# Kernel tuning notes

Measured on AMD Instinct MI355X. Metric: run time of the kernel, lower is better.

## Reference

```python
import jax, jax.numpy as jnp
import numpy as np

EMB_DIM = 128
HEAD_SIZE = 16  # embDim // numHea = 128 // 8


def setup_inputs() -> dict:
    key = jax.random.key(0)
    k1, k2, k3, k4 = jax.random.split(key, 4)
    B, T = 8, 2048
    inpEmb = jax.random.normal(k1, (B, T, EMB_DIM), dtype=jnp.float32)
    # nn.Linear(embDim, heaSiz, bias=False) weights, stored transposed so y = x @ W
    Wq = jax.random.normal(k2, (EMB_DIM, HEAD_SIZE), dtype=jnp.float32) / np.sqrt(EMB_DIM)
    Wk = jax.random.normal(k3, (EMB_DIM, HEAD_SIZE), dtype=jnp.float32) / np.sqrt(EMB_DIM)
    Wv = jax.random.normal(k4, (EMB_DIM, HEAD_SIZE), dtype=jnp.float32) / np.sqrt(EMB_DIM)
    return {"inpEmb": inpEmb, "Wq": Wq, "Wk": Wk, "Wv": Wv}


def reference(inpEmb, Wq, Wk, Wv):
    # q,k,v: [B, T, H]
    q = inpEmb @ Wq
    k = inpEmb @ Wk
    v = inpEmb @ Wv
    scale = HEAD_SIZE ** -0.5
    # scores: [B, T, T]
    scores = jnp.einsum('bqh,bkh->bqk', q, k) * scale
    T = inpEmb.shape[1]
    causal = jnp.tril(jnp.ones((T, T), dtype=bool))
    scores = jnp.where(causal, scores, -jnp.inf)
    weights = jax.nn.softmax(scores, axis=-1)
    # dropout treated as identity (eval mode) for deterministic reference
    return jnp.einsum('bqk,bkh->bqh', weights, v)
```

## Files before the change

kernel.cpp:

```cpp
#include <hip/hip_runtime.h>
#include <hip/hip_bf16.h>

#define T_SEQ 2048
#define EMB   128
#define H     16
#define BATCH 8
#define MAXP  16
#define VSTR  2064
#define SLOT  10
#define QSCALE 0.360673760222241f

#define EXP2F(x) __builtin_amdgcn_exp2f(x)

typedef short short8_t __attribute__((ext_vector_type(8)));
typedef float f32x4    __attribute__((ext_vector_type(4)));

__device__ __forceinline__ unsigned short f2bf(float f) {
    __hip_bfloat16 h = __float2bfloat16(f);
    return *reinterpret_cast<unsigned short*>(&h);
}

__global__ __launch_bounds__(256) void qkv_kernel(
    const float* __restrict__ x,
    const float* __restrict__ Wq,
    const float* __restrict__ Wk,
    const float* __restrict__ Wv,
    unsigned short* __restrict__ Qbf,
    unsigned short* __restrict__ Kbf,
    unsigned short* __restrict__ Vt)
{
    __shared__ unsigned short Wt[3][16][136];

    const int tid = threadIdx.x;
#pragma unroll
    for (int p = 0; p < 6; ++p) {
        const int idx4 = tid + p * 256;
        const int flat = idx4 * 4;
        const int mm   = flat >> 11;
        const int rem  = flat & 2047;
        const int d    = rem >> 4;
        const int c0   = rem & 15;
        const float* Wm = (mm == 0) ? Wq : (mm == 1) ? Wk : Wv;
        float4 w = *reinterpret_cast<const float4*>(Wm + rem);
        Wt[mm][c0    ][d] = f2bf(w.x);
        Wt[mm][c0 + 1][d] = f2bf(w.y);
        Wt[mm][c0 + 2][d] = f2bf(w.z);
        Wt[mm][c0 + 3][d] = f2bf(w.w);
    }
    __syncthreads();

    const int wv   = tid >> 6;
    const int lane = tid & 63;
    const int q    = lane >> 4;
    const int n    = lane & 15;
    const int row0 = blockIdx.x * 64 + wv * 16;
    const float* xr = x + (size_t)(row0 + n) * EMB;

    f32x4 aq = {0,0,0,0}, ak = {0,0,0,0}, av = {0,0,0,0};
#pragma unroll
    for (int t = 0; t < 4; ++t) {
        const int k0 = t * 32 + q * 8;
        float4 xa = *reinterpret_cast<const float4*>(xr + k0);
        float4 xb = *reinterpret_cast<const float4*>(xr + k0 + 4);
        union { unsigned short s[8]; short8_t v; } xf;
        xf.s[0]=f2bf(xa.x); xf.s[1]=f2bf(xa.y); xf.s[2]=f2bf(xa.z); xf.s[3]=f2bf(xa.w);
        xf.s[4]=f2bf(xb.x); xf.s[5]=f2bf(xb.y); xf.s[6]=f2bf(xb.z); xf.s[7]=f2bf(xb.w);
        short8_t wqf = *reinterpret_cast<const short8_t*>(&Wt[0][n][k0]);
        short8_t wkf = *reinterpret_cast<const short8_t*>(&Wt[1][n][k0]);
        short8_t wvf = *reinterpret_cast<const short8_t*>(&Wt[2][n][k0]);
        aq = __builtin_amdgcn_mfma_f32_16x16x32_bf16(xf.v, wqf, aq, 0, 0, 0);
        ak = __builtin_amdgcn_mfma_f32_16x16x32_bf16(xf.v, wkf, ak, 0, 0, 0);
        av = __builtin_amdgcn_mfma_f32_16x16x32_bf16(xf.v, wvf, av, 0, 0, 0);
    }

    const int grow = row0 + q * 4;
    const int b    = grow >> 11;
    const int ib0  = grow & 2047;
#pragma unroll
    for (int r = 0; r < 4; ++r) {
        Qbf[(size_t)(grow + r) * H + n] = f2bf(aq[r] * QSCALE);
        Kbf[(size_t)(grow + r) * H + n] = f2bf(ak[r]);
    }
    union { unsigned short s[4]; unsigned long long u; } vp;
    vp.s[0]=f2bf(av[0]); vp.s[1]=f2bf(av[1]); vp.s[2]=f2bf(av[2]); vp.s[3]=f2bf(av[3]);
    *reinterpret_cast<unsigned long long*>(
        Vt + ((size_t)b * H + n) * VSTR + ib0) = vp.u;
}

__global__ __launch_bounds__(256) void attn_phase1(
    const unsigned short* __restrict__ Qbf,
    const unsigned short* __restrict__ Kbf,
    const unsigned short* __restrict__ Vt,
    unsigned int* __restrict__ P2)
{
    __shared__ unsigned int Pbuf[4][16][68];

    int r = blockIdx.x;
    int qt = 0;
    while (r >= (qt >> 1) + 1) { r -= (qt >> 1) + 1; ++qt; }
    const int cch  = r;
    const int b    = blockIdx.y;
    const int i0   = qt << 6;
    const int j0   = cch << 7;

    const int tid  = threadIdx.x;
    const int wv   = tid >> 6;
    const int lane = tid & 63;
    const int q    = lane >> 4;
    const int n    = lane & 15;
    const int wrow0 = i0 + wv * 16;
    const int irow  = wrow0 + n;

    const unsigned short* Qp = Qbf + (size_t)b * T_SEQ * H;
    const unsigned short* Kp = Kbf + (size_t)b * T_SEQ * H;
    const unsigned short* vrow = Vt + (size_t)b * H * VSTR + (size_t)n * VSTR;

    short8_t qf = {0,0,0,0,0,0,0,0};
    if (q < 2)
        qf = *reinterpret_cast<const short8_t*>(Qp + (size_t)irow * H + q * 8);

    f32x4 S[8];
#pragma unroll
    for (int s = 0; s < 8; ++s) {
        short8_t kf = {0,0,0,0,0,0,0,0};
        if (q < 2)
            kf = *reinterpret_cast<const short8_t*>(
                    Kp + (size_t)(j0 + s * 16 + n) * H + q * 8);
        f32x4 z = {0.f, 0.f, 0.f, 0.f};
        S[s] = __builtin_amdgcn_mfma_f32_16x16x32_bf16(kf, qf, z, 0, 0, 0);
    }
    short8_t vf[4];
#pragma unroll
    for (int h = 0; h < 4; ++h)
        vf[h] = *reinterpret_cast<const short8_t*>(vrow + j0 + h * 32 + q * 8);

    float tm = -1e30f;
    if (j0 + 127 > wrow0) {
#pragma unroll
        for (int s = 0; s < 8; ++s) {
            const int kb = j0 + s * 16 + q * 4;
#pragma unroll
            for (int rr = 0; rr < 4; ++rr) {
                float v = (kb + rr <= irow) ? S[s][rr] : -1e30f;
                S[s][rr] = v;
                tm = fmaxf(tm, v);
            }
        }
    } else {
#pragma unroll
        for (int s = 0; s < 8; ++s)
            tm = fmaxf(tm, fmaxf(fmaxf(S[s][0], S[s][1]),
                                 fmaxf(S[s][2], S[s][3])));
    }
    tm = fmaxf(tm, __shfl_xor(tm, 16));
    tm = fmaxf(tm, __shfl_xor(tm, 32));
    const float m = tm;

    float l = 0.f;
#pragma unroll
    for (int s = 0; s < 8; ++s) {
        float e0 = EXP2F(S[s][0] - m);
        float e1 = EXP2F(S[s][1] - m);
        float e2 = EXP2F(S[s][2] - m);
        float e3 = EXP2F(S[s][3] - m);
        l += (e0 + e1) + (e2 + e3);
        unsigned int b0 = __builtin_bit_cast(unsigned int, e0);
        unsigned int b1 = __builtin_bit_cast(unsigned int, e1);
        unsigned int b2 = __builtin_bit_cast(unsigned int, e2);
        unsigned int b3 = __builtin_bit_cast(unsigned int, e3);
        unsigned long long pw =
            (unsigned long long)((b1 & 0xffff0000u) | (b0 >> 16)) |
            ((unsigned long long)((b3 & 0xffff0000u) | (b2 >> 16)) << 32);
        *reinterpret_cast<unsigned long long*>(&Pbuf[wv][n][8 * s + 2 * q]) = pw;
    }

    f32x4 acc = {0.f, 0.f, 0.f, 0.f};
#pragma unroll
    for (int h = 0; h < 4; ++h) {
        uint4 p4 = *reinterpret_cast<const uint4*>(&Pbuf[wv][n][16 * h + 4 * q]);
        union { uint4 u; short8_t v; } pu; pu.u = p4;
        acc = __builtin_amdgcn_mfma_f32_16x16x32_bf16(vf[h], pu.v, acc, 0, 0, 0);
    }

    l += __shfl_xor(l, 16);
    l += __shfl_xor(l, 32);

    unsigned int* pp = P2 + ((size_t)(b * T_SEQ + irow) * MAXP + cch) * SLOT;
    const unsigned int pa =
        (unsigned int)f2bf(acc[0]) | ((unsigned int)f2bf(acc[1]) << 16);
    const unsigned int pb =
        (unsigned int)f2bf(acc[2]) | ((unsigned int)f2bf(acc[3]) << 16);
    unsigned long long aw = (unsigned long long)pa |
                            ((unsigned long long)pb << 32);
    *reinterpret_cast<unsigned long long*>(pp + 2 * q) = aw;
    if (q == 0) {
        unsigned long long mlw =
            (unsigned long long)__builtin_bit_cast(unsigned int, m) |
            ((unsigned long long)__builtin_bit_cast(unsigned int, l) << 32);
        *reinterpret_cast<unsigned long long*>(pp + 8) = mlw;
    }
}

__global__ __launch_bounds__(256) void attn_phase2(
    const unsigned int* __restrict__ P2, float* __restrict__ out)
{
    const int gid = blockIdx.x * 256 + threadIdx.x;
    const int row = gid >> 4;
    const int d   = gid & 15;
    const int ib  = row & (T_SEQ - 1);
    const int nc  = (ib >> 7) + 1;
    const unsigned int* base = P2 + (size_t)row * (MAXP * SLOT);
    const int dpair = d >> 1;
    const int dhi   = (d & 1) << 4;

    float mv[MAXP];
#pragma unroll
    for (int p = 0; p < MAXP; ++p) {
        const float raw = __builtin_bit_cast(float, base[p * SLOT + 8]);
        mv[p] = (p < nc) ? raw : -1e30f;
    }
    float M = -1e30f;
#pragma unroll
    for (int p = 0; p < MAXP; ++p) M = fmaxf(M, mv[p]);

    float L = 0.f, o = 0.f;
#pragma unroll
    for (int p = 0; p < MAXP; ++p) {
        const float wgt = EXP2F(mv[p] - M);
        const float lv  = __builtin_bit_cast(float, base[p * SLOT + 9]);
        const unsigned int pr = base[p * SLOT + dpair];
        const float av = __builtin_bit_cast(float, ((pr >> dhi) & 0xffffu) << 16);
        L += wgt * lv;
        o += wgt * av;
    }
    out[gid] = o / L;
}

extern "C" void kernel_launch(void* const* d_in, const int* in_sizes, int n_in,
                              void* d_out, int out_size, void* d_ws, size_t ws_size,
                              hipStream_t stream)
{
    const float* x  = (const float*)d_in[0];
    const float* Wq = (const float*)d_in[1];
    const float* Wk = (const float*)d_in[2];
    const float* Wv = (const float*)d_in[3];
    float* out = (float*)d_out;

    const size_t NE = (size_t)BATCH * T_SEQ * H;
    unsigned short* Qbf = (unsigned short*)d_ws;
    unsigned short* Kbf = Qbf + NE;
    unsigned short* Vt  = Kbf + NE;
    unsigned int* P2 = (unsigned int*)(Vt + (size_t)BATCH * H * VSTR);

    qkv_kernel<<<BATCH * T_SEQ / 64, 256, 0, stream>>>(
        x, Wq, Wk, Wv, Qbf, Kbf, Vt);
    attn_phase1<<<dim3(272, BATCH), 256, 0, stream>>>(Qbf, Kbf, Vt, P2);
    attn_phase2<<<(int)(NE / 256), 256, 0, stream>>>(P2, out);
}
```

Baseline: 84.24 us.

## Fuse split-K attention phases into single online-softmax kernel

Replaces the two-kernel attention (per-chunk partials written to workspace, then a merge kernel) with one kernel per 64-row query tile that loops over key chunks using online softmax rescaling. This removes the partial-result workspace traffic and one kernel launch. In exchange the grid shrinks to 256 blocks with causal load imbalance, so later tiles serially process up to 16 chunks, which reduces parallelism.

```diff
diff --git a/kernel.cpp b/kernel.cpp
--- a/kernel.cpp
+++ b/kernel.cpp
@@ -5,9 +5,7 @@
 #define EMB   128
 #define H     16
 #define BATCH 8
-#define MAXP  16
 #define VSTR  2064
-#define SLOT  10
 #define QSCALE 0.360673760222241f
 
 #define EXP2F(x) __builtin_amdgcn_exp2f(x)
@@ -87,21 +85,18 @@
         Vt + ((size_t)b * H + n) * VSTR + ib0) = vp.u;
 }
 
-__global__ __launch_bounds__(256) void attn_phase1(
+__global__ __launch_bounds__(256) void attn_fused(
     const unsigned short* __restrict__ Qbf,
     const unsigned short* __restrict__ Kbf,
     const unsigned short* __restrict__ Vt,
-    unsigned int* __restrict__ P2)
+    float* __restrict__ out)
 {
     __shared__ unsigned int Pbuf[4][16][68];
 
-    int r = blockIdx.x;
-    int qt = 0;
-    while (r >= (qt >> 1) + 1) { r -= (qt >> 1) + 1; ++qt; }
-    const int cch  = r;
-    const int b    = blockIdx.y;
-    const int i0   = qt << 6;
-    const int j0   = cch << 7;
+    const int qt = blockIdx.x;
+    const int b  = blockIdx.y;
+    const int i0 = qt << 6;
+    const int nc = (qt >> 1) + 1;
 
     const int tid  = threadIdx.x;
     const int wv   = tid >> 6;
@@ -119,121 +114,92 @@
     if (q < 2)
         qf = *reinterpret_cast<const short8_t*>(Qp + (size_t)irow * H + q * 8);
 
-    f32x4 S[8];
-#pragma unroll
-    for (int s = 0; s < 8; ++s) {
-        short8_t kf = {0,0,0,0,0,0,0,0};
-        if (q < 2)
-            kf = *reinterpret_cast<const short8_t*>(
-                    Kp + (size_t)(j0 + s * 16 + n) * H + q * 8);
-        f32x4 z = {0.f, 0.f, 0.f, 0.f};
-        S[s] = __builtin_amdgcn_mfma_f32_16x16x32_bf16(kf, qf, z, 0, 0, 0);
-    }
-    short8_t vf[4];
-#pragma unroll
-    for (int h = 0; h < 4; ++h)
-        vf[h] = *reinterpret_cast<const short8_t*>(vrow + j0 + h * 32 + q * 8);
-
-    float tm = -1e30f;
-    if (j0 + 127 > wrow0) {
+    f32x4 acc = {0.f, 0.f, 0.f, 0.f};
+    float m = -1e30f;
+    float l = 0.f;
+
+    for (int c = 0; c < nc; ++c) {
+        const int j0 = c << 7;
+
+        f32x4 S[8];
 #pragma unroll
         for (int s = 0; s < 8; ++s) {
-            const int kb = j0 + s * 16 + q * 4;
-#pragma unroll
-            for (int rr = 0; rr < 4; ++rr) {
-                float v = (kb + rr <= irow) ? S[s][rr] : -1e30f;
-                S[s][rr] = v;
-                tm = fmaxf(tm, v);
+            short8_t kf = {0,0,0,0,0,0,0,0};
+            if (q < 2)
+                kf = *reinterpret_cast<const short8_t*>(
+                        Kp + (size_t)(j0 + s * 16 + n) * H + q * 8);
+            f32x4 z = {0.f, 0.f, 0.f, 0.f};
+            S[s] = __builtin_amdgcn_mfma_f32_16x16x32_bf16(kf, qf, z, 0, 0, 0);
+        }
+        short8_t vf[4];
+#pragma unroll
+        for (int h = 0; h < 4; ++h)
+            vf[h] = *reinterpret_cast<const short8_t*>(vrow + j0 + h * 32 + q * 8);
+
+        float tm = -1e30f;
+        if (j0 + 127 > wrow0) {
+#pragma unroll
+            for (int s = 0; s < 8; ++s) {
+                const int kb = j0 + s * 16 + q * 4;
+#pragma unroll
+                for (int rr = 0; rr < 4; ++rr) {
+                    float v = (kb + rr <= irow) ? S[s][rr] : -1e30f;
+                    S[s][rr] = v;
+                    tm = fmaxf(tm, v);
+                }
             }
-        }
-    } else {
-#pragma unroll
-        for (int s = 0; s < 8; ++s)
-            tm = fmaxf(tm, fmaxf(fmaxf(S[s][0], S[s][1]),
-                                 fmaxf(S[s][2], S[s][3])));
-    }
-    tm = fmaxf(tm, __shfl_xor(tm, 16));
-    tm = fmaxf(tm, __shfl_xor(tm, 32));
-    const float m = tm;
-
-    float l = 0.f;
-#pragma unroll
-    for (int s = 0; s < 8; ++s) {
-        float e0 = EXP2F(S[s][0] - m);
-        float e1 = EXP2F(S[s][1] - m);
-        float e2 = EXP2F(S[s][2] - m);
-        float e3 = EXP2F(S[s][3] - m);
-        l += (e0 + e1) + (e2 + e3);
-        unsigned int b0 = __builtin_bit_cast(unsigned int, e0);
-        unsigned int b1 = __builtin_bit_cast(unsigned int, e1);
-        unsigned int b2 = __builtin_bit_cast(unsigned int, e2);
-        unsigned int b3 = __builtin_bit_cast(unsigned int, e3);
-        unsigned long long pw =
-            (unsigned long long)((b1 & 0xffff0000u) | (b0 >> 16)) |
-            ((unsigned long long)((b3 & 0xffff0000u) | (b2 >> 16)) << 32);
-        *reinterpret_cast<unsigned long long*>(&Pbuf[wv][n][8 * s + 2 * q]) = pw;
-    }
-
-    f32x4 acc = {0.f, 0.f, 0.f, 0.f};
-#pragma unroll
-    for (int h = 0; h < 4; ++h) {
-        uint4 p4 = *reinterpret_cast<const uint4*>(&Pbuf[wv][n][16 * h + 4 * q]);
-        union { uint4 u; short8_t v; } pu; pu.u = p4;
-        acc = __builtin_amdgcn_mfma_f32_16x16x32_bf16(vf[h], pu.v, acc, 0, 0, 0);
+        } else {
+#pragma unroll
+            for (int s = 0; s < 8; ++s)
+                tm = fmaxf(tm, fmaxf(fmaxf(S[s][0], S[s][1]),
+                                     fmaxf(S[s][2], S[s][3])));
+        }
+        tm = fmaxf(tm, __shfl_xor(tm, 16));
+        tm = fmaxf(tm, __shfl_xor(tm, 32));
+
+        const float mn = fmaxf(m, tm);
+        const float rs = EXP2F(m - mn);
+        m = mn;
+        acc[0] *= rs; acc[1] *= rs; acc[2] *= rs; acc[3] *= rs;
+
+        float lc = 0.f;
+#pragma unroll
+        for (int s = 0; s < 8; ++s) {
+            float e0 = EXP2F(S[s][0] - mn);
+            float e1 = EXP2F(S[s][1] - mn);
+            float e2 = EXP2F(S[s][2] - mn);
+            float e3 = EXP2F(S[s][3] - mn);
+            lc += (e0 + e1) + (e2 + e3);
+            unsigned int b0 = __builtin_bit_cast(unsigned int, e0);
+            unsigned int b1 = __builtin_bit_cast(unsigned int, e1);
+            unsigned int b2 = __builtin_bit_cast(unsigned int, e2);
+            unsigned int b3 = __builtin_bit_cast(unsigned int, e3);
+            unsigned long long pw =
+                (unsigned long long)((b1 & 0xffff0000u) | (b0 >> 16)) |
+                ((unsigned long long)((b3 & 0xffff0000u) | (b2 >> 16)) << 32);
+            *reinterpret_cast<unsigned long long*>(&Pbuf[wv][n][8 * s + 2 * q]) = pw;
+        }
+        l = l * rs + lc;
+
+#pragma unroll
+        for (int h = 0; h < 4; ++h) {
+            uint4 p4 = *reinterpret_cast<const uint4*>(&Pbuf[wv][n][16 * h + 4 * q]);
+            union { uint4 u; short8_t v; } pu; pu.u = p4;
+            acc = __builtin_amdgcn_mfma_f32_16x16x32_bf16(vf[h], pu.v, acc, 0, 0, 0);
+        }
     }
 
     l += __shfl_xor(l, 16);
     l += __shfl_xor(l, 32);
-
-    unsigned int* pp = P2 + ((size_t)(b * T_SEQ + irow) * MAXP + cch) * SLOT;
-    const unsigned int pa =
-        (unsigned int)f2bf(acc[0]) | ((unsigned int)f2bf(acc[1]) << 16);
-    const unsigned int pb =
-        (unsigned int)f2bf(acc[2]) | ((unsigned int)f2bf(acc[3]) << 16);
-    unsigned long long aw = (unsigned long long)pa |
-                            ((unsigned long long)pb << 32);
-    *reinterpret_cast<unsigned long long*>(pp + 2 * q) = aw;
-    if (q == 0) {
-        unsigned long long mlw =
-            (unsigned long long)__builtin_bit_cast(unsigned int, m) |
-            ((unsigned long long)__builtin_bit_cast(unsigned int, l) << 32);
-        *reinterpret_cast<unsigned long long*>(pp + 8) = mlw;
-    }
-}
-
-__global__ __launch_bounds__(256) void attn_phase2(
-    const unsigned int* __restrict__ P2, float* __restrict__ out)
-{
-    const int gid = blockIdx.x * 256 + threadIdx.x;
-    const int row = gid >> 4;
-    const int d   = gid & 15;
-    const int ib  = row & (T_SEQ - 1);
-    const int nc  = (ib >> 7) + 1;
-    const unsigned int* base = P2 + (size_t)row * (MAXP * SLOT);
-    const int dpair = d >> 1;
-    const int dhi   = (d & 1) << 4;
-
-    float mv[MAXP];
-#pragma unroll
-    for (int p = 0; p < MAXP; ++p) {
-        const float raw = __builtin_bit_cast(float, base[p * SLOT + 8]);
-        mv[p] = (p < nc) ? raw : -1e30f;
-    }
-    float M = -1e30f;
-#pragma unroll
-    for (int p = 0; p < MAXP; ++p) M = fmaxf(M, mv[p]);
-
-    float L = 0.f, o = 0.f;
-#pragma unroll
-    for (int p = 0; p < MAXP; ++p) {
-        const float wgt = EXP2F(mv[p] - M);
-        const float lv  = __builtin_bit_cast(float, base[p * SLOT + 9]);
-        const unsigned int pr = base[p * SLOT + dpair];
-        const float av = __builtin_bit_cast(float, ((pr >> dhi) & 0xffffu) << 16);
-        L += wgt * lv;
-        o += wgt * av;
-    }
-    out[gid] = o / L;
+    const float inv = 1.f / l;
+
+    float4 o4;
+    o4.x = acc[0] * inv;
+    o4.y = acc[1] * inv;
+    o4.z = acc[2] * inv;
+    o4.w = acc[3] * inv;
+    *reinterpret_cast<float4*>(
+        out + ((size_t)b * T_SEQ + irow) * H + 4 * q) = o4;
 }
 
 extern "C" void kernel_launch(void* const* d_in, const int* in_sizes, int n_in,
@@ -250,10 +216,8 @@
     unsigned short* Qbf = (unsigned short*)d_ws;
     unsigned short* Kbf = Qbf + NE;
     unsigned short* Vt  = Kbf + NE;
-    unsigned int* P2 = (unsigned int*)(Vt + (size_t)BATCH * H * VSTR);
 
     qkv_kernel<<<BATCH * T_SEQ / 64, 256, 0, stream>>>(
         x, Wq, Wk, Wv, Qbf, Kbf, Vt);
-    attn_phase1<<<dim3(272, BATCH), 256, 0, stream>>>(Qbf, Kbf, Vt, P2);
-    attn_phase2<<<(int)(NE / 256), 256, 0, stream>>>(P2, out);
-}
+    attn_fused<<<dim3(32, BATCH), 256, 0, stream>>>(Qbf, Kbf, Vt, out);
+}
```

Result: slower. 110.4 us (+31.1%).
